# Performance work log

Hardware: AMD Instinct MI355X
Metric: run time of the kernel (lower is better)

The kernel has to match this reference:

```python
import jax, jax.numpy as jnp
import numpy as np

T = 200000
N_LIMBS = 49
N_POINTS = 50
N_BONES = 20
EPS = 1e-10
REG_RATES = (0.001, 0.1)
# binary-tree skeleton: child b has parent (b-1)//2, bone-length index (b-1)%N_BONES
STRUCTURE = [((b - 1) // 2, b, (b - 1) % N_BONES) for b in range(1, N_POINTS)]

def _path_matrix():
    # P[b, i] = 1 if limb i lies on the root->node-b path. Then node position =
    # root + deltas @ P.T, which is exactly the sequential tree accumulation
    # x[b] = x[a] + delta_i of the original torch loop, vectorized.
    P = np.zeros((N_POINTS, N_LIMBS), dtype=np.float32)
    for i, (a, b, l) in enumerate(STRUCTURE):
        P[b] = P[a]
        P[b, i] = 1.0
    return P

PATH_T = jnp.asarray(_path_matrix().T)  # (n_limbs, n_points)
BONE_IDX = jnp.asarray(np.array([l for (_, _, l) in STRUCTURE], dtype=np.int32))


def setup_inputs() -> dict:
    key = jax.random.key(0)
    ks = jax.random.split(key, 10)
    f = jnp.float32
    return {
        "lines": jax.random.normal(ks[0], (N_BONES,), f) * 0.1,
        "rootsx": jax.random.normal(ks[1], (T, 1), f),
        "rootsy": jax.random.normal(ks[2], (T, 1), f),
        "rootsz": jax.random.normal(ks[3], (T, 1), f),
        "anglesx": jax.random.normal(ks[4], (T, N_LIMBS), f),
        "anglesy": jax.random.normal(ks[5], (T, N_LIMBS), f),
        "anglesz": jax.random.normal(ks[6], (T, N_LIMBS), f),
        "tarx_values": jax.random.normal(ks[7], (T, N_POINTS), f),
        "tary_values": jax.random.normal(ks[8], (T, N_POINTS), f),
        "w_values": jax.random.uniform(ks[9], (T, N_POINTS), f),
    }


def reference(lines, rootsx, rootsy, rootsz, anglesx, anglesy, anglesz,
              tarx_values, tary_values, w_values):
    # per-limb bone length L = exp(lines[l])  -> (n_limbs,)
    L = jnp.exp(lines)[BONE_IDX]
    normA = jnp.sqrt(anglesx ** 2 + anglesy ** 2 + anglesz ** 2) + EPS  # (T, n_limbs)
    dx = L * anglesx / normA
    dy = L * anglesy / normA
    dz = L * anglesz / normA
    # accumulate deltas along root->node paths (equivalent to the torch tree loop)
    x = rootsx + dx @ PATH_T  # (T, n_points); node 0 column is just the root
    y = rootsy + dy @ PATH_T
    z = rootsz + dz @ PATH_T
    loss = jnp.sum(w_values * (x - tarx_values) ** 2
                   + w_values * (y - tary_values) ** 2) / (T * N_POINTS)
    reg1 = jnp.sum(jnp.exp(lines))
    tdx = x[:-1] - x[1:]
    tdy = y[:-1] - y[1:]
    tdz = z[:-1] - z[1:]
    reg2 = jnp.sum(tdx ** 2 + tdy ** 2 + tdz ** 2) / ((T - 1) * N_POINTS)
    total_loss = loss + REG_RATES[0] * reg1 + REG_RATES[1] * reg2
    return x, y, z, total_loss
```

## Files before the change

### kernel.cpp

```cpp
#include <hip/hip_runtime.h>

#define T_TOTAL 200000
#define NL 49
#define NP 50
#define NB 20
#define THREADS 256
#define WPB 4
#define TPW 8
#define NWAVES (T_TOTAL / TPW)
#define NBLOCKS (NWAVES / WPB)

__global__ __launch_bounds__(THREADS, 5) void bbf_fused(
    const float* __restrict__ lines,
    const float* __restrict__ rootsx,
    const float* __restrict__ rootsy,
    const float* __restrict__ rootsz,
    const float* __restrict__ ax,
    const float* __restrict__ ay,
    const float* __restrict__ az,
    const float* __restrict__ tarx,
    const float* __restrict__ tary,
    const float* __restrict__ w,
    float* __restrict__ outx,
    float* __restrict__ outy,
    float* __restrict__ outz,
    double* __restrict__ partials)
{
    __shared__ double redL[WPB], redR[WPB];

    const int tid  = threadIdx.x;
    const int lane = tid & 63;
    const int wix  = tid >> 6;
    const int gw   = blockIdx.x * WPB + wix;
    const int tw   = __builtin_amdgcn_readfirstlane(gw * TPW);
    const bool lastw = (tw + TPW) >= T_TOTAL;

    const bool isNode = (lane < NP);
    const bool isLimb = (lane >= 1 && lane < NP);
    const int  li = isLimb ? (lane - 1) : 0;
    const int  lc = isNode ? lane : (NP - 1);

    const float Lv = isLimb ? expf(lines[li % NB]) : 0.f;

    const int a1 = isLimb ? ((lane - 1) >> 1) : 0;
    const int a2 = (a1 > 0) ? ((a1 - 1) >> 1) : 0;
    const int a3 = (a2 > 0) ? ((a2 - 1) >> 1) : 0;
    const int a4 = (a3 > 0) ? ((a3 - 1) >> 1) : 0;

    const float* axp = ax + (size_t)tw * NL + li;
    const float* ayp = ay + (size_t)tw * NL + li;
    const float* azp = az + (size_t)tw * NL + li;
    const size_t o8 = lastw ? (size_t)(7 * NL) : (size_t)(8 * NL);
    float ax0,ay0,az0,ax1,ay1,az1,ax2,ay2,az2,ax3,ay3,az3,ax4,ay4,az4,
          ax5,ay5,az5,ax6,ay6,az6,ax7,ay7,az7,ax8,ay8,az8;
    ax0=axp[0*NL]; ay0=ayp[0*NL]; az0=azp[0*NL];
    ax1=axp[1*NL]; ay1=ayp[1*NL]; az1=azp[1*NL];
    ax2=axp[2*NL]; ay2=ayp[2*NL]; az2=azp[2*NL];
    ax3=axp[3*NL]; ay3=ayp[3*NL]; az3=azp[3*NL];
    ax4=axp[4*NL]; ay4=ayp[4*NL]; az4=azp[4*NL];
    ax5=axp[5*NL]; ay5=ayp[5*NL]; az5=azp[5*NL];
    ax6=axp[6*NL]; ay6=ayp[6*NL]; az6=azp[6*NL];
    ax7=axp[7*NL]; ay7=ayp[7*NL]; az7=azp[7*NL];
    ax8=axp[o8];   ay8=ayp[o8];   az8=azp[o8];

    const float* txp = tarx + (size_t)tw * NP + lc;
    const float* typ = tary + (size_t)tw * NP + lc;
    const float* wp  = w    + (size_t)tw * NP + lc;
    const float tx0=txp[0*NP], ty0=typ[0*NP], q0=wp[0*NP];
    const float tx1=txp[1*NP], ty1=typ[1*NP], q1=wp[1*NP];
    const float tx2=txp[2*NP], ty2=typ[2*NP], q2=wp[2*NP];
    const float tx3=txp[3*NP], ty3=typ[3*NP], q3=wp[3*NP];
    const float tx4=txp[4*NP], ty4=typ[4*NP], q4=wp[4*NP];
    const float tx5=txp[5*NP], ty5=typ[5*NP], q5=wp[5*NP];
    const float tx6=txp[6*NP], ty6=typ[6*NP], q6=wp[6*NP];
    const float tx7=txp[7*NP], ty7=typ[7*NP], q7=wp[7*NP];

    asm volatile("" ::
        "v"(ax0),"v"(ay0),"v"(az0),"v"(ax1),"v"(ay1),"v"(az1),
        "v"(ax2),"v"(ay2),"v"(az2),"v"(ax3),"v"(ay3),"v"(az3),
        "v"(ax4),"v"(ay4),"v"(az4),"v"(ax5),"v"(ay5),"v"(az5),
        "v"(ax6),"v"(ay6),"v"(az6),"v"(ax7),"v"(ay7),"v"(az7),
        "v"(ax8),"v"(ay8),"v"(az8));
    asm volatile("" ::
        "v"(tx0),"v"(ty0),"v"(q0),"v"(tx1),"v"(ty1),"v"(q1),
        "v"(tx2),"v"(ty2),"v"(q2),"v"(tx3),"v"(ty3),"v"(q3),
        "v"(tx4),"v"(ty4),"v"(q4),"v"(tx5),"v"(ty5),"v"(q5),
        "v"(tx6),"v"(ty6),"v"(q6),"v"(tx7),"v"(ty7),"v"(q7));

    const int tH = lastw ? (tw + TPW - 1) : (tw + TPW);
    const float rx0=rootsx[tw+0], ry0=rootsy[tw+0], rz0=rootsz[tw+0];
    const float rx1=rootsx[tw+1], ry1=rootsy[tw+1], rz1=rootsz[tw+1];
    const float rx2=rootsx[tw+2], ry2=rootsy[tw+2], rz2=rootsz[tw+2];
    const float rx3=rootsx[tw+3], ry3=rootsy[tw+3], rz3=rootsz[tw+3];
    const float rx4=rootsx[tw+4], ry4=rootsy[tw+4], rz4=rootsz[tw+4];
    const float rx5=rootsx[tw+5], ry5=rootsy[tw+5], rz5=rootsz[tw+5];
    const float rx6=rootsx[tw+6], ry6=rootsy[tw+6], rz6=rootsz[tw+6];
    const float rx7=rootsx[tw+7], ry7=rootsy[tw+7], rz7=rootsz[tw+7];
    const float rx8=rootsx[tH],   ry8=rootsy[tH],   rz8=rootsz[tH];

    float* oxp = outx + (size_t)tw * NP + lane;
    float* oyp = outy + (size_t)tw * NP + lane;
    float* ozp = outz + (size_t)tw * NP + lane;

    float lossAcc = 0.f, regAcc = 0.f;

#define CHAIN(K, AXK, AYK, AZK)                                               \
    float X##K, Y##K, Z##K;                                                   \
    {                                                                         \
        const float n = sqrtf(AXK*AXK + AYK*AYK + AZK*AZK) + 1e-10f;          \
        const float s = Lv / n;                                               \
        float dx = AXK * s, dy = AYK * s, dz = AZK * s;                       \
        dx += __shfl(dx, a1); dy += __shfl(dy, a1); dz += __shfl(dz, a1);     \
        dx += __shfl(dx, a2); dy += __shfl(dy, a2); dz += __shfl(dz, a2);     \
        dx += __shfl(dx, a4); dy += __shfl(dy, a4); dz += __shfl(dz, a4);     \
        X##K = dx + rx##K;                                                    \
        Y##K = dy + ry##K;                                                    \
        Z##K = dz + rz##K;                                                    \
    }
#define EMIT(K)                                                               \
    if (isNode) {                                                             \
        oxp[(K)*NP] = X##K; oyp[(K)*NP] = Y##K; ozp[(K)*NP] = Z##K;           \
        const float ex = X##K - tx##K, ey = Y##K - ty##K;                     \
        lossAcc += q##K * (ex * ex + ey * ey);                                \
    }
#define REG2(KP, K)                                                           \
    if (isNode) {                                                             \
        const float d1 = X##KP - X##K, d2 = Y##KP - Y##K, d3 = Z##KP - Z##K;  \
        regAcc += d1 * d1 + d2 * d2 + d3 * d3;                                \
    }

    CHAIN(0, ax0, ay0, az0) EMIT(0)
    CHAIN(1, ax1, ay1, az1) EMIT(1) REG2(0, 1)
    CHAIN(2, ax2, ay2, az2) EMIT(2) REG2(1, 2)
    CHAIN(3, ax3, ay3, az3) EMIT(3) REG2(2, 3)
    CHAIN(4, ax4, ay4, az4) EMIT(4) REG2(3, 4)
    CHAIN(5, ax5, ay5, az5) EMIT(5) REG2(4, 5)
    CHAIN(6, ax6, ay6, az6) EMIT(6) REG2(5, 6)
    CHAIN(7, ax7, ay7, az7) EMIT(7) REG2(6, 7)
    if (!lastw) {
        CHAIN(8, ax8, ay8, az8)
        REG2(7, 8)
    }
#undef CHAIN
#undef EMIT
#undef REG2

    for (int off = 32; off > 0; off >>= 1) {
        lossAcc += __shfl_down(lossAcc, off);
        regAcc  += __shfl_down(regAcc, off);
    }
    if (lane == 0) { redL[wix] = (double)lossAcc; redR[wix] = (double)regAcc; }
    __syncthreads();
    if (tid == 0) {
        double l = 0.0, r = 0.0;
        for (int i = 0; i < WPB; ++i) { l += redL[i]; r += redR[i]; }
        partials[2 * (size_t)blockIdx.x]     = l;
        partials[2 * (size_t)blockIdx.x + 1] = r;
    }
}

__global__ __launch_bounds__(1024) void bbf_finalize(
    const float* __restrict__ lines,
    const double* __restrict__ partials,
    float* __restrict__ out_total)
{
    __shared__ double rl[16], rr[16];
    const int tid = threadIdx.x;
    double l = 0.0, r = 0.0;
    for (int i = tid; i < NBLOCKS; i += 1024) {
        l += partials[2 * (size_t)i];
        r += partials[2 * (size_t)i + 1];
    }
    for (int off = 32; off > 0; off >>= 1) {
        l += __shfl_down(l, off);
        r += __shfl_down(r, off);
    }
    const int wid = tid >> 6;
    if ((tid & 63) == 0) { rl[wid] = l; rr[wid] = r; }
    __syncthreads();
    if (tid == 0) {
        double L = 0.0, R = 0.0;
        for (int i = 0; i < 16; ++i) { L += rl[i]; R += rr[i]; }
        double reg1 = 0.0;
        for (int i = 0; i < NB; ++i) reg1 += (double)expf(lines[i]);
        const double loss = L / ((double)T_TOTAL * (double)NP);
        const double reg2 = R / ((double)(T_TOTAL - 1) * (double)NP);
        *out_total = (float)(loss + 0.001 * reg1 + 0.1 * reg2);
    }
}

extern "C" void kernel_launch(void* const* d_in, const int* in_sizes, int n_in,
                              void* d_out, int out_size, void* d_ws, size_t ws_size,
                              hipStream_t stream) {
    const float* lines  = (const float*)d_in[0];
    const float* rootsx = (const float*)d_in[1];
    const float* rootsy = (const float*)d_in[2];
    const float* rootsz = (const float*)d_in[3];
    const float* ax     = (const float*)d_in[4];
    const float* ay     = (const float*)d_in[5];
    const float* az     = (const float*)d_in[6];
    const float* tarx   = (const float*)d_in[7];
    const float* tary   = (const float*)d_in[8];
    const float* w      = (const float*)d_in[9];

    float* out = (float*)d_out;
    const size_t plane = (size_t)T_TOTAL * NP;
    float* outx = out;
    float* outy = out + plane;
    float* outz = out + 2 * plane;
    float* out_total = out + 3 * plane;

    double* partials = (double*)d_ws;

    bbf_fused<<<NBLOCKS, THREADS, 0, stream>>>(
        lines, rootsx, rootsy, rootsz, ax, ay, az, tarx, tary, w,
        outx, outy, outz, partials);
    bbf_finalize<<<1, 1024, 0, stream>>>(lines, partials, out_total);
}
```

Before: 76.72 us.

## Stage wave results in LDS and use vectorized float4 global traffic

Each wave now writes its computed x/y/z node positions into shared memory instead of storing them straight to global memory. It then reads them back as float4 to issue contiguous 16-byte stores, and loads tarx/tary/w as float4 over the wave's flat 8x50 tile. The loss and temporal-difference terms are computed from the LDS tile, using neighbouring-row offsets in place of per-lane register pairs. This aims to replace partially filled 50-lane scalar accesses with fully coalesced vector accesses and to free the registers that held preloaded targets, at the cost of about 22KB of LDS per block plus extra LDS round trips.

```diff
diff --git a/kernel.cpp b/kernel.cpp
--- a/kernel.cpp
+++ b/kernel.cpp
@@ -9,6 +9,7 @@
 #define TPW 8
 #define NWAVES (T_TOTAL / TPW)
 #define NBLOCKS (NWAVES / WPB)
+#define REG 456
 
 __global__ __launch_bounds__(THREADS, 5) void bbf_fused(
     const float* __restrict__ lines,
@@ -26,6 +27,9 @@
     float* __restrict__ outz,
     double* __restrict__ partials)
 {
+    __shared__ __align__(16) float xsW[WPB][REG];
+    __shared__ __align__(16) float ysW[WPB][REG];
+    __shared__ __align__(16) float zsW[WPB][REG];
     __shared__ double redL[WPB], redR[WPB];
 
     const int tid  = threadIdx.x;
@@ -38,7 +42,6 @@
     const bool isNode = (lane < NP);
     const bool isLimb = (lane >= 1 && lane < NP);
     const int  li = isLimb ? (lane - 1) : 0;
-    const int  lc = isNode ? lane : (NP - 1);
 
     const float Lv = isLimb ? expf(lines[li % NB]) : 0.f;
 
@@ -62,30 +65,12 @@
     ax6=axp[6*NL]; ay6=ayp[6*NL]; az6=azp[6*NL];
     ax7=axp[7*NL]; ay7=ayp[7*NL]; az7=azp[7*NL];
     ax8=axp[o8];   ay8=ayp[o8];   az8=azp[o8];
-
-    const float* txp = tarx + (size_t)tw * NP + lc;
-    const float* typ = tary + (size_t)tw * NP + lc;
-    const float* wp  = w    + (size_t)tw * NP + lc;
-    const float tx0=txp[0*NP], ty0=typ[0*NP], q0=wp[0*NP];
-    const float tx1=txp[1*NP], ty1=typ[1*NP], q1=wp[1*NP];
-    const float tx2=txp[2*NP], ty2=typ[2*NP], q2=wp[2*NP];
-    const float tx3=txp[3*NP], ty3=typ[3*NP], q3=wp[3*NP];
-    const float tx4=txp[4*NP], ty4=typ[4*NP], q4=wp[4*NP];
-    const float tx5=txp[5*NP], ty5=typ[5*NP], q5=wp[5*NP];
-    const float tx6=txp[6*NP], ty6=typ[6*NP], q6=wp[6*NP];
-    const float tx7=txp[7*NP], ty7=typ[7*NP], q7=wp[7*NP];
-
     asm volatile("" ::
         "v"(ax0),"v"(ay0),"v"(az0),"v"(ax1),"v"(ay1),"v"(az1),
         "v"(ax2),"v"(ay2),"v"(az2),"v"(ax3),"v"(ay3),"v"(az3),
         "v"(ax4),"v"(ay4),"v"(az4),"v"(ax5),"v"(ay5),"v"(az5),
         "v"(ax6),"v"(ay6),"v"(az6),"v"(ax7),"v"(ay7),"v"(az7),
         "v"(ax8),"v"(ay8),"v"(az8));
-    asm volatile("" ::
-        "v"(tx0),"v"(ty0),"v"(q0),"v"(tx1),"v"(ty1),"v"(q1),
-        "v"(tx2),"v"(ty2),"v"(q2),"v"(tx3),"v"(ty3),"v"(q3),
-        "v"(tx4),"v"(ty4),"v"(q4),"v"(tx5),"v"(ty5),"v"(q5),
-        "v"(tx6),"v"(ty6),"v"(q6),"v"(tx7),"v"(ty7),"v"(q7));
 
     const int tH = lastw ? (tw + TPW - 1) : (tw + TPW);
     const float rx0=rootsx[tw+0], ry0=rootsy[tw+0], rz0=rootsz[tw+0];
@@ -98,14 +83,11 @@
     const float rx7=rootsx[tw+7], ry7=rootsy[tw+7], rz7=rootsz[tw+7];
     const float rx8=rootsx[tH],   ry8=rootsy[tH],   rz8=rootsz[tH];
 
-    float* oxp = outx + (size_t)tw * NP + lane;
-    float* oyp = outy + (size_t)tw * NP + lane;
-    float* ozp = outz + (size_t)tw * NP + lane;
-
-    float lossAcc = 0.f, regAcc = 0.f;
+    float* xw = xsW[wix];
+    float* yw = ysW[wix];
+    float* zw = zsW[wix];
 
 #define CHAIN(K, AXK, AYK, AZK)                                               \
-    float X##K, Y##K, Z##K;                                                   \
     {                                                                         \
         const float n = sqrtf(AXK*AXK + AYK*AYK + AZK*AZK) + 1e-10f;          \
         const float s = Lv / n;                                               \
@@ -113,37 +95,73 @@
         dx += __shfl(dx, a1); dy += __shfl(dy, a1); dz += __shfl(dz, a1);     \
         dx += __shfl(dx, a2); dy += __shfl(dy, a2); dz += __shfl(dz, a2);     \
         dx += __shfl(dx, a4); dy += __shfl(dy, a4); dz += __shfl(dz, a4);     \
-        X##K = dx + rx##K;                                                    \
-        Y##K = dy + ry##K;                                                    \
-        Z##K = dz + rz##K;                                                    \
-    }
-#define EMIT(K)                                                               \
-    if (isNode) {                                                             \
-        oxp[(K)*NP] = X##K; oyp[(K)*NP] = Y##K; ozp[(K)*NP] = Z##K;           \
-        const float ex = X##K - tx##K, ey = Y##K - ty##K;                     \
-        lossAcc += q##K * (ex * ex + ey * ey);                                \
-    }
-#define REG2(KP, K)                                                           \
-    if (isNode) {                                                             \
-        const float d1 = X##KP - X##K, d2 = Y##KP - Y##K, d3 = Z##KP - Z##K;  \
-        regAcc += d1 * d1 + d2 * d2 + d3 * d3;                                \
-    }
-
-    CHAIN(0, ax0, ay0, az0) EMIT(0)
-    CHAIN(1, ax1, ay1, az1) EMIT(1) REG2(0, 1)
-    CHAIN(2, ax2, ay2, az2) EMIT(2) REG2(1, 2)
-    CHAIN(3, ax3, ay3, az3) EMIT(3) REG2(2, 3)
-    CHAIN(4, ax4, ay4, az4) EMIT(4) REG2(3, 4)
-    CHAIN(5, ax5, ay5, az5) EMIT(5) REG2(4, 5)
-    CHAIN(6, ax6, ay6, az6) EMIT(6) REG2(5, 6)
-    CHAIN(7, ax7, ay7, az7) EMIT(7) REG2(6, 7)
-    if (!lastw) {
-        CHAIN(8, ax8, ay8, az8)
-        REG2(7, 8)
-    }
+        if (isNode) {                                                         \
+            xw[(K)*NP + lane] = dx + rx##K;                                   \
+            yw[(K)*NP + lane] = dy + ry##K;                                   \
+            zw[(K)*NP + lane] = dz + rz##K;                                   \
+        }                                                                     \
+    }
+    CHAIN(0, ax0, ay0, az0)
+    CHAIN(1, ax1, ay1, az1)
+    CHAIN(2, ax2, ay2, az2)
+    CHAIN(3, ax3, ay3, az3)
+    CHAIN(4, ax4, ay4, az4)
+    CHAIN(5, ax5, ay5, az5)
+    CHAIN(6, ax6, ay6, az6)
+    CHAIN(7, ax7, ay7, az7)
+    CHAIN(8, ax8, ay8, az8)
 #undef CHAIN
-#undef EMIT
-#undef REG2
+
+    const size_t gb = (size_t)tw * NP;
+    const float4* tx4 = (const float4*)(tarx + gb);
+    const float4* ty4 = (const float4*)(tary + gb);
+    const float4* qw4 = (const float4*)(w + gb);
+    float4* ox4 = (float4*)(outx + gb);
+    float4* oy4 = (float4*)(outy + gb);
+    float4* oz4 = (float4*)(outz + gb);
+
+    float lossAcc = 0.f, regAcc = 0.f;
+#pragma unroll
+    for (int it = 0; it < 2; ++it) {
+        const int c = lane + it * 64;
+        if (c < (TPW * NP) / 4) {
+            const int j = c << 2;
+            const float4 X  = *(const float4*)&xw[j];
+            const float4 Y  = *(const float4*)&yw[j];
+            const float4 Z  = *(const float4*)&zw[j];
+            ox4[c] = X;
+            oy4[c] = Y;
+            oz4[c] = Z;
+            const float4 TX = tx4[c];
+            const float4 TY = ty4[c];
+            const float4 WV = qw4[c];
+            const float4 XA = *(const float4*)&xw[j + 48];
+            const float4 XB = *(const float4*)&xw[j + 52];
+            const float4 YA = *(const float4*)&yw[j + 48];
+            const float4 YB = *(const float4*)&yw[j + 52];
+            const float4 ZA = *(const float4*)&zw[j + 48];
+            const float4 ZB = *(const float4*)&zw[j + 52];
+            const float xv[4] = {X.x, X.y, X.z, X.w};
+            const float yv[4] = {Y.x, Y.y, Y.z, Y.w};
+            const float zv[4] = {Z.x, Z.y, Z.z, Z.w};
+            const float tx[4] = {TX.x, TX.y, TX.z, TX.w};
+            const float ty[4] = {TY.x, TY.y, TY.z, TY.w};
+            const float qv[4] = {WV.x, WV.y, WV.z, WV.w};
+            const float xn[4] = {XA.z, XA.w, XB.x, XB.y};
+            const float yn[4] = {YA.z, YA.w, YB.x, YB.y};
+            const float zn[4] = {ZA.z, ZA.w, ZB.x, ZB.y};
+#pragma unroll
+            for (int e = 0; e < 4; ++e) {
+                const float ex = xv[e] - tx[e];
+                const float ey = yv[e] - ty[e];
+                lossAcc += qv[e] * (ex * ex + ey * ey);
+                const float d1 = xv[e] - xn[e];
+                const float d2 = yv[e] - yn[e];
+                const float d3 = zv[e] - zn[e];
+                regAcc += d1 * d1 + d2 * d2 + d3 * d3;
+            }
+        }
+    }
 
     for (int off = 32; off > 0; off >>= 1) {
         lossAcc += __shfl_down(lossAcc, off);
```

New measurement: 76.17 us. Within noise of the previous version (-0.7%).
